# Optimization experiments

Hardware: AMD Instinct MI355X
Metric: run time of the kernel (lower is better)

The kernel has to match this reference:

```python
import jax, jax.numpy as jnp
import numpy as np

B, T, D, H = 64, 2048, 256, 256

def setup_inputs() -> dict:
    key = jax.random.key(0)
    k_x, k_z, k_r, k_h = jax.random.split(key, 4)
    gate_in = D + H
    # lecun_normal: std = 1/sqrt(fan_in)
    s = 1.0 / np.sqrt(gate_in)
    return {
        "x": jax.random.normal(k_x, (B, T, D), dtype=jnp.float32),
        "W_z": jax.random.normal(k_z, (gate_in, H), dtype=jnp.float32) * s,
        "b_z": jnp.zeros((H,), dtype=jnp.float32),
        "W_r": jax.random.normal(k_r, (gate_in, H), dtype=jnp.float32) * s,
        "b_r": jnp.zeros((H,), dtype=jnp.float32),
        "W_h": jax.random.normal(k_h, (gate_in, H), dtype=jnp.float32) * s,
        "b_h": jnp.zeros((H,), dtype=jnp.float32),
    }

def reference(x, W_z, b_z, W_r, b_r, W_h, b_h):
    Bx, Tx, Dx = x.shape
    Hx = W_z.shape[1]

    def scan_fn(h_prev, x_t):
        xh = jnp.concatenate([x_t, h_prev], axis=-1)        # [B, D+H]
        z = jax.nn.sigmoid(xh @ W_z + b_z)                   # [B, H]
        r = jax.nn.sigmoid(xh @ W_r + b_r)                   # [B, H]
        xrh = jnp.concatenate([x_t, r * h_prev], axis=-1)   # [B, D+H]
        h_hat = jnp.tanh(xrh @ W_h + b_h)                    # [B, H]
        h_new = (1 - z) * h_prev + z * h_hat
        return h_new, h_new

    h0 = jnp.zeros((Bx, Hx), dtype=x.dtype)
    x_t = jnp.transpose(x, (1, 0, 2))                        # [T, B, D]
    _, all_h = jax.lax.scan(scan_fn, h0, x_t)                # [T, B, H]
    return jnp.transpose(all_h, (1, 0, 2))                   # [B, T, H]
```

## Files before the change

kernel.cpp:

```cpp
#include <hip/hip_runtime.h>

typedef _Float16 half2_t __attribute__((ext_vector_type(2)));

#define NB 64
#define NT 2048
#define ND 256
#define NH 256
#define NTHR 512
#define CHUNK 32
#define NCHUNK (NT / CHUNK)

#define XT_STRIDE 132
#define LDS_DW (32 * XT_STRIDE + 16)
#define VQ_BYTE 256

__device__ __forceinline__ float sigmoid_f(float x) { return 1.f / (1.f + __expf(-x)); }
__device__ __forceinline__ float tanh_f(float x)    { return 1.f - 2.f / (1.f + __expf(2.f * x)); }
__device__ __forceinline__ half2_t mkh2(float a, float b) {
    half2_t r; r.x = (_Float16)a; r.y = (_Float16)b; return r;
}
__device__ __forceinline__ half2_t u2h2(unsigned u) { return __builtin_bit_cast(half2_t, u); }
__device__ __forceinline__ float h2get(unsigned u, int idx) {
    half2_t h = u2h2(u);
    return idx ? (float)h.y : (float)h.x;
}
__device__ __forceinline__ int dot4i8(unsigned a, unsigned b, int c) {
#if __has_builtin(__builtin_amdgcn_sdot4)
    return __builtin_amdgcn_sdot4((int)a, (int)b, c, false);
#else
    int d;
    asm("v_dot4_i32_i8 %0, %1, %2, %3" : "=v"(d) : "v"(a), "v"(b), "v"(c));
    return d;
#endif
}
#define BAR_LDS() asm volatile("s_waitcnt lgkmcnt(0)\n\ts_barrier" ::: "memory")

extern "C" __global__ void __launch_bounds__(NTHR)
gru_fused(const float* __restrict__ x,
          const float* __restrict__ Wz, const float* __restrict__ bz,
          const float* __restrict__ Wr, const float* __restrict__ br,
          const float* __restrict__ Wh, const float* __restrict__ bh,
          float* __restrict__ out,
          unsigned* prodflag, unsigned* consflag,
          unsigned long long* preZR, unsigned* preH, int ring)
{
    __shared__ __align__(16) unsigned smem[LDS_DW];
    const int tid = threadIdx.x;
    const int bid = blockIdx.x;
    const int rmask = ring - 1;
    const int c  = tid >> 1;
    const int kh = tid & 1;

    if (bid >= NB) {
        const int pb = bid - NB;
        const int g  = pb >> 6;
        const int b  = pb & 63;
        const float* W    = (g == 0) ? Wz : (g == 1) ? Wr : Wh;
        const float* bias = (g == 0) ? bz : (g == 1) ? br : bh;

        half2_t w2[64];
        #pragma unroll
        for (int j = 0; j < 64; ++j)
            w2[j] = mkh2(W[(kh * 128 + 2 * j) * NH + c],
                         W[(kh * 128 + 2 * j + 1) * NH + c]);
        const float bv = bias[c];

        for (int ch = 0; ch < NCHUNK; ++ch) {
            const int lead = ch * CHUNK + CHUNK - ring;
            if (lead > 0) {
                if (tid == 0) {
                    unsigned it = 0;
                    while ((int)__hip_atomic_load(&consflag[b], __ATOMIC_RELAXED,
                                                  __HIP_MEMORY_SCOPE_AGENT) < lead) {
                        __builtin_amdgcn_s_sleep(8);
                        if (++it > (1u << 20)) break;
                    }
                }
                __syncthreads();
            }
            const int t0 = ch * CHUNK;
            {
                const float4* xs = reinterpret_cast<const float4*>(
                    x + (size_t)b * NT * ND + (size_t)t0 * ND);
                #pragma unroll
                for (int rep = 0; rep < 4; ++rep) {
                    const int f = rep * NTHR + tid;
                    const float4 v = xs[f];
                    const int tt = f >> 6;
                    const int u2 = f & 63;
                    uint2 pk;
                    pk.x = __builtin_bit_cast(unsigned, mkh2(v.x, v.y));
                    pk.y = __builtin_bit_cast(unsigned, mkh2(v.z, v.w));
                    *reinterpret_cast<uint2*>(&smem[tt * XT_STRIDE + u2 * 2]) = pk;
                }
            }
            __syncthreads();
            #pragma unroll 1
            for (int t = 0; t < CHUNK; ++t) {
                const uint4* xr4 = reinterpret_cast<const uint4*>(
                    &smem[t * XT_STRIDE + kh * 64]);
                float a0 = 0.f, a1 = 0.f, a2 = 0.f, a3 = 0.f;
                #pragma unroll
                for (int i = 0; i < 16; ++i) {
                    const uint4 xv = xr4[i];
                    a0 = __builtin_amdgcn_fdot2(u2h2(xv.x), w2[i*4+0], a0, false);
                    a1 = __builtin_amdgcn_fdot2(u2h2(xv.y), w2[i*4+1], a1, false);
                    a2 = __builtin_amdgcn_fdot2(u2h2(xv.z), w2[i*4+2], a2, false);
                    a3 = __builtin_amdgcn_fdot2(u2h2(xv.w), w2[i*4+3], a3, false);
                }
                float a = (a0 + a1) + (a2 + a3);
                a += __shfl_xor(a, 1, 64);
                a += bv;
                const float an = __shfl_xor(a, 2, 64);
                if (!(tid & 3)) {
                    const unsigned pk = __builtin_bit_cast(unsigned, mkh2(a, an));
                    const size_t slot = (size_t)b * ring + ((t0 + t) & rmask);
                    if (g == 2) {
                        __hip_atomic_store(&preH[slot * 128 + (c >> 1)], pk,
                                           __ATOMIC_RELAXED, __HIP_MEMORY_SCOPE_AGENT);
                    } else {
                        unsigned* zr32 = reinterpret_cast<unsigned*>(&preZR[slot * 128 + (c >> 1)]);
                        __hip_atomic_store(&zr32[g], pk,
                                           __ATOMIC_RELAXED, __HIP_MEMORY_SCOPE_AGENT);
                    }
                }
            }
            asm volatile("s_waitcnt vmcnt(0)" ::: "memory");
            __syncthreads();
            if (tid == 0)
                __hip_atomic_store(&prodflag[b * 3 + g], (unsigned)(ch + 1),
                                   __ATOMIC_RELAXED, __HIP_MEMORY_SCOPE_AGENT);
            __syncthreads();
        }
        return;
    }

    const int b   = bid;
    const int sub = c & 1;
    const int kb  = ND + kh * 128;

    float mxz = 1e-8f, mxr = 1e-8f, mxh = 1e-8f;
    #pragma unroll
    for (int j = 0; j < 128; ++j) {
        mxz = fmaxf(mxz, fabsf(Wz[(kb + j) * NH + c]));
        mxr = fmaxf(mxr, fabsf(Wr[(kb + j) * NH + c]));
        mxh = fmaxf(mxh, fabsf(Wh[(kb + j) * NH + c]));
    }
    const float qsz = 127.0f / mxz, qsr = 127.0f / mxr, qsh = 127.0f / mxh;
    const float deqz = mxz / (127.0f * 127.0f);
    const float deqr = mxr / (127.0f * 127.0f);
    const float deqh = mxh / (127.0f * 127.0f);

    uint4 wz4[8], wr4[8], wh4[8];
    #pragma unroll
    for (int i = 0; i < 8; ++i) {
        unsigned dz[4], dr[4], dh[4];
        #pragma unroll
        for (int d = 0; d < 4; ++d) {
            unsigned az = 0, ar = 0, ah = 0;
            #pragma unroll
            for (int j = 0; j < 4; ++j) {
                const int k = (i * 4 + d) * 4 + j;
                const int qz = __float2int_rn(Wz[(kb + k) * NH + c] * qsz);
                const int qr = __float2int_rn(Wr[(kb + k) * NH + c] * qsr);
                const int qh = __float2int_rn(Wh[(kb + k) * NH + c] * qsh);
                az |= ((unsigned)(qz & 255)) << (8 * j);
                ar |= ((unsigned)(qr & 255)) << (8 * j);
                ah |= ((unsigned)(qh & 255)) << (8 * j);
            }
            dz[d] = az; dr[d] = ar; dh[d] = ah;
        }
        wz4[i] = make_uint4(dz[0], dz[1], dz[2], dz[3]);
        wr4[i] = make_uint4(dr[0], dr[1], dr[2], dr[3]);
        wh4[i] = make_uint4(dh[0], dh[1], dh[2], dh[3]);
    }

    if (tid < 128) smem[tid] = 0u;
    float hreg = 0.f;

    if (tid < 3) {
        unsigned it = 0;
        while (__hip_atomic_load(&prodflag[b * 3 + tid], __ATOMIC_RELAXED,
                                 __HIP_MEMORY_SCOPE_AGENT) < 1u) {
            __builtin_amdgcn_s_sleep(8);
            if (++it > (1u << 20)) break;
        }
    }
    __syncthreads();

    const unsigned long long* zrb = preZR + (size_t)b * ring * 128 + (c >> 1);
    const unsigned*           hhb = preH  + (size_t)b * ring * 128 + (c >> 1);
    float* outb = out + (size_t)b * NT * NH + c;
    const uint4* hq4 = reinterpret_cast<const uint4*>(smem) + kh * 8;
    const uint4* vq4 = reinterpret_cast<const uint4*>(
                           reinterpret_cast<const char*>(smem) + VQ_BYTE) + kh * 8;
    char* hqb = reinterpret_cast<char*>(smem);

    unsigned long long zr_c = __hip_atomic_load(zrb, __ATOMIC_RELAXED, __HIP_MEMORY_SCOPE_AGENT);
    unsigned           hh_c = __hip_atomic_load(hhb, __ATOMIC_RELAXED, __HIP_MEMORY_SCOPE_AGENT);

    #pragma unroll 1
    for (int t = 0; t < NT; ++t) {
        const int tn = t + 1;
        const bool pf = (tn < NT) && ((tn & (CHUNK - 1)) != 0);
        unsigned long long zr_n = 0; unsigned hh_n = 0;
        if (pf) {
            const int so = (tn & rmask) * 128;
            zr_n = __hip_atomic_load(zrb + so, __ATOMIC_RELAXED, __HIP_MEMORY_SCOPE_AGENT);
            hh_n = __hip_atomic_load(hhb + so, __ATOMIC_RELAXED, __HIP_MEMORY_SCOPE_AGENT);
        }

        int az0 = 0, az1 = 0, ar0 = 0, ar1 = 0;
        #pragma unroll
        for (int i = 0; i < 8; ++i) {
            const uint4 hv = hq4[i];
            const uint4 wz = wz4[i], wr = wr4[i];
            az0 = dot4i8(hv.x, wz.x, az0); az1 = dot4i8(hv.y, wz.y, az1);
            az0 = dot4i8(hv.z, wz.z, az0); az1 = dot4i8(hv.w, wz.w, az1);
            ar0 = dot4i8(hv.x, wr.x, ar0); ar1 = dot4i8(hv.y, wr.y, ar1);
            ar0 = dot4i8(hv.z, wr.z, ar0); ar1 = dot4i8(hv.w, wr.w, ar1);
        }
        float azf = (float)(az0 + az1) * deqz;
        float arf = (float)(ar0 + ar1) * deqr;
        azf += __shfl_xor(azf, 1, 64);
        arf += __shfl_xor(arf, 1, 64);
        const float z = sigmoid_f(azf + h2get((unsigned)(zr_c & 0xffffffffu), sub));
        const float r = sigmoid_f(arf + h2get((unsigned)(zr_c >> 32), sub));
        const float v = r * hreg;
        if (kh == 0)
            hqb[VQ_BYTE + c] = (char)__float2int_rn(v * 127.0f);
        BAR_LDS();

        int ah0 = 0, ah1 = 0;
        #pragma unroll
        for (int i = 0; i < 8; ++i) {
            const uint4 vv = vq4[i];
            const uint4 wh = wh4[i];
            ah0 = dot4i8(vv.x, wh.x, ah0); ah1 = dot4i8(vv.y, wh.y, ah1);
            ah0 = dot4i8(vv.z, wh.z, ah0); ah1 = dot4i8(vv.w, wh.w, ah1);
        }
        float ahf = (float)(ah0 + ah1) * deqh;
        ahf += __shfl_xor(ahf, 1, 64);
        const float hhat = tanh_f(ahf + h2get(hh_c, sub));
        const float hn = hreg + z * (hhat - hreg);
        hreg = hn;
        if (kh == 0) {
            outb[(size_t)t * NH] = hn;
            hqb[c] = (char)__float2int_rn(hn * 127.0f);
        }
        BAR_LDS();

        if (pf) {
            zr_c = zr_n; hh_c = hh_n;
        } else if (tn < NT) {
            if (tid == 0)
                __hip_atomic_store(&consflag[b], (unsigned)tn,
                                   __ATOMIC_RELAXED, __HIP_MEMORY_SCOPE_AGENT);
            const unsigned need = (unsigned)((tn >> 5) + 1);
            if (tid < 3) {
                unsigned it = 0;
                while (__hip_atomic_load(&prodflag[b * 3 + tid], __ATOMIC_RELAXED,
                                         __HIP_MEMORY_SCOPE_AGENT) < need) {
                    __builtin_amdgcn_s_sleep(8);
                    if (++it > (1u << 20)) break;
                }
            }
            __syncthreads();
            const int so = (tn & rmask) * 128;
            zr_c = __hip_atomic_load(zrb + so, __ATOMIC_RELAXED, __HIP_MEMORY_SCOPE_AGENT);
            hh_c = __hip_atomic_load(hhb + so, __ATOMIC_RELAXED, __HIP_MEMORY_SCOPE_AGENT);
        }
    }
}

extern "C" void kernel_launch(void* const* d_in, const int* in_sizes, int n_in,
                              void* d_out, int out_size, void* d_ws, size_t ws_size,
                              hipStream_t stream) {
    const float* x  = (const float*)d_in[0];
    const float* Wz = (const float*)d_in[1];
    const float* bz = (const float*)d_in[2];
    const float* Wr = (const float*)d_in[3];
    const float* br = (const float*)d_in[4];
    const float* Wh = (const float*)d_in[5];
    const float* bh = (const float*)d_in[6];
    float* outp = (float*)d_out;

    const size_t base = 4096;
    int ring = 32;
    for (int r = 2048; r >= 32; r >>= 1) {
        const size_t need = base + (size_t)NB * r * 128 * 12;
        if (need <= ws_size) { ring = r; break; }
    }
    char* w = (char*)d_ws;
    unsigned* prodflag = (unsigned*)w;
    unsigned* consflag = (unsigned*)(w + 1024);
    unsigned long long* preZR = (unsigned long long*)(w + base);
    unsigned* preH = (unsigned*)(w + base + (size_t)NB * ring * 128 * 8);

    hipMemsetAsync(w, 0, 4096, stream);
    gru_fused<<<256, NTHR, 0, stream>>>(x, Wz, bz, Wr, br, Wh, bh, outp,
                                        prodflag, consflag, preZR, preH, ring);
}
```

Baseline: 2.214 ms.

## Halve block size: one thread per hidden unit with readlane broadcast of h

Consumer blocks now use 256 threads, each owning a full output column with all 256 recurrent int8 weights in registers. This removes the cross-lane K-split shuffle reductions. The quantized h and r*h vectors are read once per lane from LDS and broadcast with readlane instead of every thread issuing 8 uint4 LDS reads. Producer blocks likewise compute two columns per thread so each LDS x read feeds twice the work. The cost is higher register pressure (48 uint4 weight registers per consumer thread, 128 half2 per producer thread) and fewer threads to hide the serial latency of each step.

```diff
diff --git a/kernel.cpp b/kernel.cpp
--- a/kernel.cpp
+++ b/kernel.cpp
@@ -6,13 +6,12 @@
 #define NT 2048
 #define ND 256
 #define NH 256
-#define NTHR 512
+#define NTHR 256
 #define CHUNK 32
 #define NCHUNK (NT / CHUNK)
 
 #define XT_STRIDE 132
 #define LDS_DW (32 * XT_STRIDE + 16)
-#define VQ_BYTE 256
 
 __device__ __forceinline__ float sigmoid_f(float x) { return 1.f / (1.f + __expf(-x)); }
 __device__ __forceinline__ float tanh_f(float x)    { return 1.f - 2.f / (1.f + __expf(2.f * x)); }
@@ -24,9 +23,9 @@
     half2_t h = u2h2(u);
     return idx ? (float)h.y : (float)h.x;
 }
-__device__ __forceinline__ int dot4i8(unsigned a, unsigned b, int c) {
+__device__ __forceinline__ int dot4i8(int a, int b, int c) {
 #if __has_builtin(__builtin_amdgcn_sdot4)
-    return __builtin_amdgcn_sdot4((int)a, (int)b, c, false);
+    return __builtin_amdgcn_sdot4(a, b, c, false);
 #else
     int d;
     asm("v_dot4_i32_i8 %0, %1, %2, %3" : "=v"(d) : "v"(a), "v"(b), "v"(c));
@@ -48,8 +47,6 @@
     const int tid = threadIdx.x;
     const int bid = blockIdx.x;
     const int rmask = ring - 1;
-    const int c  = tid >> 1;
-    const int kh = tid & 1;
 
     if (bid >= NB) {
         const int pb = bid - NB;
@@ -57,13 +54,18 @@
         const int b  = pb & 63;
         const float* W    = (g == 0) ? Wz : (g == 1) ? Wr : Wh;
         const float* bias = (g == 0) ? bz : (g == 1) ? br : bh;
-
-        half2_t w2[64];
+        const int kh = tid & 1;
+        const int c2 = tid >> 1;
+        const int c0 = c2 * 2, c1 = c0 + 1;
+
+        half2_t wa[64], wb[64];
         #pragma unroll
-        for (int j = 0; j < 64; ++j)
-            w2[j] = mkh2(W[(kh * 128 + 2 * j) * NH + c],
-                         W[(kh * 128 + 2 * j + 1) * NH + c]);
-        const float bv = bias[c];
+        for (int j = 0; j < 64; ++j) {
+            const int k = kh * 128 + 2 * j;
+            wa[j] = mkh2(W[k * NH + c0], W[(k + 1) * NH + c0]);
+            wb[j] = mkh2(W[k * NH + c1], W[(k + 1) * NH + c1]);
+        }
+        const float bv0 = bias[c0], bv1 = bias[c1];
 
         for (int ch = 0; ch < NCHUNK; ++ch) {
             const int lead = ch * CHUNK + CHUNK - ring;
@@ -83,7 +85,7 @@
                 const float4* xs = reinterpret_cast<const float4*>(
                     x + (size_t)b * NT * ND + (size_t)t0 * ND);
                 #pragma unroll
-                for (int rep = 0; rep < 4; ++rep) {
+                for (int rep = 0; rep < 8; ++rep) {
                     const int f = rep * NTHR + tid;
                     const float4 v = xs[f];
                     const int tt = f >> 6;
@@ -99,27 +101,31 @@
             for (int t = 0; t < CHUNK; ++t) {
                 const uint4* xr4 = reinterpret_cast<const uint4*>(
                     &smem[t * XT_STRIDE + kh * 64]);
-                float a0 = 0.f, a1 = 0.f, a2 = 0.f, a3 = 0.f;
+                float a00 = 0.f, a01 = 0.f, a10 = 0.f, a11 = 0.f;
                 #pragma unroll
                 for (int i = 0; i < 16; ++i) {
                     const uint4 xv = xr4[i];
-                    a0 = __builtin_amdgcn_fdot2(u2h2(xv.x), w2[i*4+0], a0, false);
-                    a1 = __builtin_amdgcn_fdot2(u2h2(xv.y), w2[i*4+1], a1, false);
-                    a2 = __builtin_amdgcn_fdot2(u2h2(xv.z), w2[i*4+2], a2, false);
-                    a3 = __builtin_amdgcn_fdot2(u2h2(xv.w), w2[i*4+3], a3, false);
-                }
-                float a = (a0 + a1) + (a2 + a3);
-                a += __shfl_xor(a, 1, 64);
-                a += bv;
-                const float an = __shfl_xor(a, 2, 64);
-                if (!(tid & 3)) {
-                    const unsigned pk = __builtin_bit_cast(unsigned, mkh2(a, an));
+                    a00 = __builtin_amdgcn_fdot2(u2h2(xv.x), wa[i*4+0], a00, false);
+                    a01 = __builtin_amdgcn_fdot2(u2h2(xv.y), wa[i*4+1], a01, false);
+                    a00 = __builtin_amdgcn_fdot2(u2h2(xv.z), wa[i*4+2], a00, false);
+                    a01 = __builtin_amdgcn_fdot2(u2h2(xv.w), wa[i*4+3], a01, false);
+                    a10 = __builtin_amdgcn_fdot2(u2h2(xv.x), wb[i*4+0], a10, false);
+                    a11 = __builtin_amdgcn_fdot2(u2h2(xv.y), wb[i*4+1], a11, false);
+                    a10 = __builtin_amdgcn_fdot2(u2h2(xv.z), wb[i*4+2], a10, false);
+                    a11 = __builtin_amdgcn_fdot2(u2h2(xv.w), wb[i*4+3], a11, false);
+                }
+                float a0 = a00 + a01, a1 = a10 + a11;
+                a0 += __shfl_xor(a0, 1, 64);
+                a1 += __shfl_xor(a1, 1, 64);
+                a0 += bv0; a1 += bv1;
+                if (kh == 0) {
+                    const unsigned pk = __builtin_bit_cast(unsigned, mkh2(a0, a1));
                     const size_t slot = (size_t)b * ring + ((t0 + t) & rmask);
                     if (g == 2) {
-                        __hip_atomic_store(&preH[slot * 128 + (c >> 1)], pk,
+                        __hip_atomic_store(&preH[slot * 128 + c2], pk,
                                            __ATOMIC_RELAXED, __HIP_MEMORY_SCOPE_AGENT);
                     } else {
-                        unsigned* zr32 = reinterpret_cast<unsigned*>(&preZR[slot * 128 + (c >> 1)]);
+                        unsigned* zr32 = reinterpret_cast<unsigned*>(&preZR[slot * 128 + c2]);
                         __hip_atomic_store(&zr32[g], pk,
                                            __ATOMIC_RELAXED, __HIP_MEMORY_SCOPE_AGENT);
                     }
@@ -135,35 +141,36 @@
         return;
     }
 
-    const int b   = bid;
-    const int sub = c & 1;
-    const int kb  = ND + kh * 128;
+    const int b    = bid;
+    const int c    = tid;
+    const int lane = tid & 63;
+    const int sub  = c & 1;
 
     float mxz = 1e-8f, mxr = 1e-8f, mxh = 1e-8f;
-    #pragma unroll
-    for (int j = 0; j < 128; ++j) {
-        mxz = fmaxf(mxz, fabsf(Wz[(kb + j) * NH + c]));
-        mxr = fmaxf(mxr, fabsf(Wr[(kb + j) * NH + c]));
-        mxh = fmaxf(mxh, fabsf(Wh[(kb + j) * NH + c]));
+    #pragma unroll 4
+    for (int j = 0; j < 256; ++j) {
+        mxz = fmaxf(mxz, fabsf(Wz[(ND + j) * NH + c]));
+        mxr = fmaxf(mxr, fabsf(Wr[(ND + j) * NH + c]));
+        mxh = fmaxf(mxh, fabsf(Wh[(ND + j) * NH + c]));
     }
     const float qsz = 127.0f / mxz, qsr = 127.0f / mxr, qsh = 127.0f / mxh;
     const float deqz = mxz / (127.0f * 127.0f);
     const float deqr = mxr / (127.0f * 127.0f);
     const float deqh = mxh / (127.0f * 127.0f);
 
-    uint4 wz4[8], wr4[8], wh4[8];
+    uint4 wz4[16], wr4[16], wh4[16];
     #pragma unroll
-    for (int i = 0; i < 8; ++i) {
+    for (int i = 0; i < 16; ++i) {
         unsigned dz[4], dr[4], dh[4];
         #pragma unroll
         for (int d = 0; d < 4; ++d) {
             unsigned az = 0, ar = 0, ah = 0;
             #pragma unroll
             for (int j = 0; j < 4; ++j) {
-                const int k = (i * 4 + d) * 4 + j;
-                const int qz = __float2int_rn(Wz[(kb + k) * NH + c] * qsz);
-                const int qr = __float2int_rn(Wr[(kb + k) * NH + c] * qsr);
-                const int qh = __float2int_rn(Wh[(kb + k) * NH + c] * qsh);
+                const int k = ND + (i * 4 + d) * 4 + j;
+                const int qz = __float2int_rn(Wz[k * NH + c] * qsz);
+                const int qr = __float2int_rn(Wr[k * NH + c] * qsr);
+                const int qh = __float2int_rn(Wh[k * NH + c] * qsh);
                 az |= ((unsigned)(qz & 255)) << (8 * j);
                 ar |= ((unsigned)(qr & 255)) << (8 * j);
                 ah |= ((unsigned)(qh & 255)) << (8 * j);
@@ -191,10 +198,8 @@
     const unsigned long long* zrb = preZR + (size_t)b * ring * 128 + (c >> 1);
     const unsigned*           hhb = preH  + (size_t)b * ring * 128 + (c >> 1);
     float* outb = out + (size_t)b * NT * NH + c;
-    const uint4* hq4 = reinterpret_cast<const uint4*>(smem) + kh * 8;
-    const uint4* vq4 = reinterpret_cast<const uint4*>(
-                           reinterpret_cast<const char*>(smem) + VQ_BYTE) + kh * 8;
-    char* hqb = reinterpret_cast<char*>(smem);
+    const uint4* lds4 = reinterpret_cast<const uint4*>(smem);
+    char* ldsb = reinterpret_cast<char*>(smem);
 
     unsigned long long zr_c = __hip_atomic_load(zrb, __ATOMIC_RELAXED, __HIP_MEMORY_SCOPE_AGENT);
     unsigned           hh_c = __hip_atomic_load(hhb, __ATOMIC_RELAXED, __HIP_MEMORY_SCOPE_AGENT);
@@ -210,44 +215,51 @@
             hh_n = __hip_atomic_load(hhb + so, __ATOMIC_RELAXED, __HIP_MEMORY_SCOPE_AGENT);
         }
 
-        int az0 = 0, az1 = 0, ar0 = 0, ar1 = 0;
+        const uint4 hvec = lds4[lane & 15];
+        int az0 = 0, az1 = 0, az2 = 0, az3 = 0;
+        int ar0 = 0, ar1 = 0, ar2 = 0, ar3 = 0;
         #pragma unroll
-        for (int i = 0; i < 8; ++i) {
-            const uint4 hv = hq4[i];
-            const uint4 wz = wz4[i], wr = wr4[i];
-            az0 = dot4i8(hv.x, wz.x, az0); az1 = dot4i8(hv.y, wz.y, az1);
-            az0 = dot4i8(hv.z, wz.z, az0); az1 = dot4i8(hv.w, wz.w, az1);
-            ar0 = dot4i8(hv.x, wr.x, ar0); ar1 = dot4i8(hv.y, wr.y, ar1);
-            ar0 = dot4i8(hv.z, wr.z, ar0); ar1 = dot4i8(hv.w, wr.w, ar1);
-        }
-        float azf = (float)(az0 + az1) * deqz;
-        float arf = (float)(ar0 + ar1) * deqr;
-        azf += __shfl_xor(azf, 1, 64);
-        arf += __shfl_xor(arf, 1, 64);
+        for (int i = 0; i < 16; ++i) {
+            const int sx = __builtin_amdgcn_readlane((int)hvec.x, i);
+            const int sy = __builtin_amdgcn_readlane((int)hvec.y, i);
+            const int sz = __builtin_amdgcn_readlane((int)hvec.z, i);
+            const int sw = __builtin_amdgcn_readlane((int)hvec.w, i);
+            az0 = dot4i8(sx, (int)wz4[i].x, az0);
+            az1 = dot4i8(sy, (int)wz4[i].y, az1);
+            az2 = dot4i8(sz, (int)wz4[i].z, az2);
+            az3 = dot4i8(sw, (int)wz4[i].w, az3);
+            ar0 = dot4i8(sx, (int)wr4[i].x, ar0);
+            ar1 = dot4i8(sy, (int)wr4[i].y, ar1);
+            ar2 = dot4i8(sz, (int)wr4[i].z, ar2);
+            ar3 = dot4i8(sw, (int)wr4[i].w, ar3);
+        }
+        const float azf = (float)((az0 + az1) + (az2 + az3)) * deqz;
+        const float arf = (float)((ar0 + ar1) + (ar2 + ar3)) * deqr;
         const float z = sigmoid_f(azf + h2get((unsigned)(zr_c & 0xffffffffu), sub));
         const float r = sigmoid_f(arf + h2get((unsigned)(zr_c >> 32), sub));
         const float v = r * hreg;
-        if (kh == 0)
-            hqb[VQ_BYTE + c] = (char)__float2int_rn(v * 127.0f);
+        ldsb[256 + c] = (char)__float2int_rn(v * 127.0f);
         BAR_LDS();
 
-        int ah0 = 0, ah1 = 0;
+        const uint4 vvec = lds4[16 + (lane & 15)];
+        int ah0 = 0, ah1 = 0, ah2 = 0, ah3 = 0;
         #pragma unroll
-        for (int i = 0; i < 8; ++i) {
-            const uint4 vv = vq4[i];
-            const uint4 wh = wh4[i];
-            ah0 = dot4i8(vv.x, wh.x, ah0); ah1 = dot4i8(vv.y, wh.y, ah1);
-            ah0 = dot4i8(vv.z, wh.z, ah0); ah1 = dot4i8(vv.w, wh.w, ah1);
-        }
-        float ahf = (float)(ah0 + ah1) * deqh;
-        ahf += __shfl_xor(ahf, 1, 64);
+        for (int i = 0; i < 16; ++i) {
+            const int sx = __builtin_amdgcn_readlane((int)vvec.x, i);
+            const int sy = __builtin_amdgcn_readlane((int)vvec.y, i);
+            const int sz = __builtin_amdgcn_readlane((int)vvec.z, i);
+            const int sw = __builtin_amdgcn_readlane((int)vvec.w, i);
+            ah0 = dot4i8(sx, (int)wh4[i].x, ah0);
+            ah1 = dot4i8(sy, (int)wh4[i].y, ah1);
+            ah2 = dot4i8(sz, (int)wh4[i].z, ah2);
+            ah3 = dot4i8(sw, (int)wh4[i].w, ah3);
+        }
+        const float ahf = (float)((ah0 + ah1) + (ah2 + ah3)) * deqh;
         const float hhat = tanh_f(ahf + h2get(hh_c, sub));
         const float hn = hreg + z * (hhat - hreg);
         hreg = hn;
-        if (kh == 0) {
-            outb[(size_t)t * NH] = hn;
-            hqb[c] = (char)__float2int_rn(hn * 127.0f);
-        }
+        outb[(size_t)t * NH] = hn;
+        ldsb[c] = (char)__float2int_rn(hn * 127.0f);
         BAR_LDS();
 
         if (pf) {
```

New measurement: 2.063 ms. -6.8%, faster.
